# Kernel tuning notes

Hardware: AMD Instinct MI355X
Metric: run time of the kernel (lower is better)

Reference implementation:

```python
import jax, jax.numpy as jnp
import numpy as np

B, T, NF, C = 4, 512, 65, 128
NH, E, H, DOWN, L = 4, 8, 256, 4, 100
VD = C // NH

def _ln(x, g, b, eps=1e-5):
    m = x.mean(-1, keepdims=True)
    v = ((x - m) ** 2).mean(-1, keepdims=True)
    return (x - m) / jnp.sqrt(v + eps) * g + b

def _prelu(x, a):
    return jnp.where(x >= 0, x, a * x)

def _lstm(x, h0, c0, wih, whh, bih, bhh):
    # x: [N, S, D] -> ([N, S, H], hT, cT); PyTorch gate order i,f,g,o
    xp = x @ wih.T + (bih + bhh)
    def step(carry, xt):
        h, c = carry
        g = xt + h @ whh.T
        i, f, gg, o = jnp.split(g, 4, axis=-1)
        c = jax.nn.sigmoid(f) * c + jax.nn.sigmoid(i) * jnp.tanh(gg)
        h = jax.nn.sigmoid(o) * jnp.tanh(c)
        return (h, c), h
    (hT, cT), ys = jax.lax.scan(step, (h0, c0), xp.transpose(1, 0, 2))
    return ys.transpose(1, 0, 2), hT, cT

def setup_inputs():
    key = jax.random.key(0)
    ks = iter(jax.random.split(key, 64))
    def w(*shape):
        return (jax.random.normal(next(ks), shape) * 0.05).astype(jnp.float32)
    z = lambda *s: jnp.zeros(s, jnp.float32)
    o = lambda *s: jnp.ones(s, jnp.float32)
    a = jnp.float32(0.25)  # PReLU init
    return dict(
        x=jax.random.normal(next(ks), (B, T, NF, C), jnp.float32),
        conv_w=w(C, C, DOWN), conv_b=z(C), conv_a=a, ln0_g=o(C), ln0_b=z(C),
        iwih_f=w(4*H, C), iwhh_f=w(4*H, H), ibih_f=z(4*H), ibhh_f=z(4*H),
        iwih_r=w(4*H, C), iwhh_r=w(4*H, H), ibih_r=z(4*H), ibhh_r=z(4*H),
        deconv_w=w(2*H, C, DOWN), deconv_b=z(C),
        ln1_g=o(C), ln1_b=z(C),
        wih=w(4*H, C), whh=w(4*H, H), bih=z(4*H), bhh=z(4*H),
        lin_w=w(C, H), lin_b=z(C),
        q_w=w(E*NH, C), q_b=z(E*NH), q_a=a, q_lg=o(NF*E), q_lb=z(NF*E),
        k_w=w(E*NH, C), k_b=z(E*NH), k_a=a, k_lg=o(NF*E), k_lb=z(NF*E),
        v_w=w(VD*NH, C), v_b=z(VD*NH), v_a=a, v_lg=o(NF*VD), v_lb=z(NF*VD),
        p_w=w(C, C), p_b=z(C), p_a=a, p_lg=o(NF*C), p_lb=z(NF*C),
        K_buf=z(B*NH, L-1, NF*E), V_buf=z(B*NH, L-1, NF*VD),
        h0=z(B*NF, H), c0=z(B*NF, H),
    )

def reference(x, conv_w, conv_b, conv_a, ln0_g, ln0_b,
              iwih_f, iwhh_f, ibih_f, ibhh_f, iwih_r, iwhh_r, ibih_r, ibhh_r,
              deconv_w, deconv_b, ln1_g, ln1_b, wih, whh, bih, bhh, lin_w, lin_b,
              q_w, q_b, q_a, q_lg, q_lb, k_w, k_b, k_a, k_lg, k_lb,
              v_w, v_b, v_a, v_lg, v_lb, p_w, p_b, p_a, p_lg, p_lb,
              K_buf, V_buf, h0, c0):
    Qd = NF // DOWN
    BT = B * T
    # ---- intra: Conv1d(k=s=DOWN) -> PReLU -> LN -> BiLSTM over freq -> ConvTranspose1d, residual ----
    # k == s: conv is a blocked einsum; torch drops the trailing NF - Qd*DOWN samples
    xc = x.reshape(BT, NF, C)[:, :Qd*DOWN, :].reshape(BT, Qd, DOWN, C)
    h = _prelu(jnp.einsum('nimc,ocm->nio', xc, conv_w) + conv_b, conv_a)
    h = _ln(h, ln0_g, ln0_b)
    z0 = jnp.zeros((BT, H), x.dtype)
    yf, _, _ = _lstm(h, z0, z0, iwih_f, iwhh_f, ibih_f, ibhh_f)
    yr, _, _ = _lstm(h[:, ::-1], z0, z0, iwih_r, iwhh_r, ibih_r, ibhh_r)
    hbi = jnp.concatenate([yf, yr[:, ::-1]], -1)                      # [BT, Qd, 2H]
    # ConvTranspose1d with k == s: blocked einsum; output_padding fills zeros (+bias) at the end
    zz = jnp.einsum('nid,dom->nimo', hbi, deconv_w).reshape(BT, Qd*DOWN, C)
    zz = jnp.pad(zz, ((0, 0), (0, NF - Qd*DOWN), (0, 0))) + deconv_b
    intra = zz.reshape(B, T, NF, C) + x
    # ---- inter: LN -> causal LSTM over time with carried (h0, c0) -> Linear, residual ----
    y = _ln(intra, ln1_g, ln1_b).transpose(0, 2, 1, 3).reshape(B*NF, T, C)
    ys, _, _ = _lstm(y, h0, c0, wih, whh, bih, bhh)
    y = (ys @ lin_w.T + lin_b).reshape(B, NF, T, C).transpose(0, 2, 1, 3)
    inter = y + intra
    # ---- causal sliding-window MHA with streaming K/V buffers ----
    def qkv(w_, b_, a_, lg_, lb_, d):
        hh = _prelu(jnp.einsum('btqc,dc->btqd', inter, w_) + b_, a_)
        hh = hh.reshape(B, T, NF, NH, d).transpose(0, 3, 1, 2, 4).reshape(B*NH, T, NF*d)
        return _ln(hh, lg_, lb_)
    Qh = qkv(q_w, q_b, q_a, q_lg, q_lb, E)      # [B*NH, T, NF*E]
    Kh = qkv(k_w, k_b, k_a, k_lg, k_lb, E)
    Vh = qkv(v_w, v_b, v_a, v_lg, v_lb, VD)     # [B*NH, T, NF*VD]
    Kf = jnp.concatenate([K_buf, Kh], 1)        # [B*NH, T+L-1, NF*E]
    Vf = jnp.concatenate([V_buf, Vh], 1)
    scores = jnp.einsum('bte,bse->bts', Qh, Kf) / jnp.asarray(NF*E, x.dtype)**0.5
    tq = jnp.arange(T)[:, None]
    tk = jnp.arange(T + L - 1)[None, :]
    band = (tk >= tq) & (tk < tq + L)           # window of L keys ending at frame t
    probs = jax.nn.softmax(jnp.where(band, scores, -jnp.inf), -1)
    av = jnp.einsum('bts,bsv->btv', probs, Vf)
    av = av.reshape(B, NH, T, NF, VD).transpose(0, 2, 3, 1, 4).reshape(B, T, NF, C)
    ph = _prelu(jnp.einsum('btqc,dc->btqd', av, p_w) + p_b, p_a)
    ph = _ln(ph.reshape(B, T, NF*C), p_lg, p_lb).reshape(B, T, NF, C)
    return ph + inter
```

## Files before the change

### kernel.cpp

```cpp
#include <hip/hip_runtime.h>
#include <hip/hip_bf16.h>


typedef unsigned short u16;
typedef unsigned int u32;

#define OFF_A    0ULL
#define OFF_B    68157440ULL
#define OFF_C    136314880ULL
#define OFF_DE   204472320ULL
#define OFF_WT   238551040ULL

__device__ __forceinline__ float b2f(u16 u) {
  union { u32 i; float f; } v; v.i = ((u32)u) << 16; return v.f;
}
__device__ __forceinline__ float bflo(u32 u) {
  union { u32 i; float f; } v; v.i = u << 16; return v.f;
}
__device__ __forceinline__ float bfhi(u32 u) {
  union { u32 i; float f; } v; v.i = u & 0xffff0000u; return v.f;
}
__device__ __forceinline__ float sigf(float x) { return 1.f / (1.f + __expf(-x)); }
__device__ __forceinline__ float tanh_(float x) {
  float cx = fminf(15.f, fmaxf(-15.f, x));
  float e = __expf(2.f * cx);
  return (e - 1.f) / (e + 1.f);
}
__device__ __forceinline__ void wavered2(float& s, float& q) {
  #pragma unroll
  for (int o = 32; o > 0; o >>= 1) {
    s += __shfl_down(s, o, 64);
    q += __shfl_down(q, o, 64);
  }
}

__global__ void k_transpose_ff(const float* __restrict__ src, float* __restrict__ dst,
                               int R, int K) {
  int e = blockIdx.x * 256 + threadIdx.x;
  if (e >= R * K) return;
  int r = e / K, k = e - r * K;
  dst[k * R + r] = src[e];
}

__global__ void k_transpose_fb(const float* __restrict__ src, u16* __restrict__ dst,
                               int R, int K) {
  int e = blockIdx.x * 256 + threadIdx.x;
  if (e >= R * K) return;
  int r = e / K, k = e - r * K;
  __hip_bfloat16 h = __float2bfloat16(src[e]);
  dst[k * R + r] = *(u16*)&h;
}

__global__ void k_cast_fb(const float* __restrict__ src, u16* __restrict__ dst, int n) {
  int e = blockIdx.x * 256 + threadIdx.x;
  if (e >= n) return;
  __hip_bfloat16 h = __float2bfloat16(src[e]);
  dst[e] = *(u16*)&h;
}

__global__ __launch_bounds__(256) void k_conv_ln0(
    const float* __restrict__ x32, const float* __restrict__ cw,
    const float* __restrict__ cb, const float* __restrict__ ca,
    const float* __restrict__ g0, const float* __restrict__ b0,
    float* __restrict__ hc) {
  __shared__ float xs[8192];
  __shared__ float hs[2048];
  __shared__ float mu_[16], ri_[16];
  int n = blockIdx.x, tid = threadIdx.x;
  const float4* xr = (const float4*)(x32 + (size_t)n * 8320);
  for (int e = tid; e < 2048; e += 256) ((float4*)xs)[e] = xr[e];
  __syncthreads();
  int g = tid >> 7, o = tid & 127;
  float a = ca[0];
  float cbv = cb[o];
  float acc[8];
  #pragma unroll
  for (int j = 0; j < 8; ++j) acc[j] = cbv;
  const float4* cw4 = (const float4*)cw;
  for (int c = 0; c < 128; ++c) {
    float4 w = cw4[o * 128 + c];
    #pragma unroll
    for (int j = 0; j < 8; ++j) {
      int i = 8 * g + j;
      const float* xi = &xs[i * 512 + c];
      acc[j] += w.x * xi[0] + w.y * xi[128] + w.z * xi[256] + w.w * xi[384];
    }
  }
  #pragma unroll
  for (int j = 0; j < 8; ++j) {
    int i = 8 * g + j;
    float v = acc[j];
    v = v >= 0.f ? v : a * v;
    hs[i * 128 + o] = v;
  }
  __syncthreads();
  if (tid < 16) {
    float s = 0.f, q = 0.f;
    for (int c = 0; c < 128; ++c) { float v = hs[tid * 128 + c]; s += v; q += v * v; }
    float mu = s / 128.f;
    mu_[tid] = mu;
    ri_[tid] = rsqrtf(fmaxf(q / 128.f - mu * mu, 0.f) + 1e-5f);
  }
  __syncthreads();
  float gg = g0[o], bb = b0[o];
  #pragma unroll
  for (int j = 0; j < 8; ++j) {
    int i = 8 * g + j;
    hc[((size_t)n * 16 + i) * 128 + o] = (hs[i * 128 + o] - mu_[i]) * ri_[i] * gg + bb;
  }
}

__global__ __launch_bounds__(256) void k_intra_lstm(
    const float* __restrict__ hc,
    const float* __restrict__ wiTf, const float* __restrict__ whTf,
    const float* __restrict__ bihf, const float* __restrict__ bhhf,
    const float* __restrict__ wiTr, const float* __restrict__ whTr,
    const float* __restrict__ bihr, const float* __restrict__ bhhr,
    float* __restrict__ yf, float* __restrict__ yr) {
  __shared__ float xt[1024];
  __shared__ float hsh[2048];
  __shared__ float csh[2048];
  __shared__ float gbuf[8192];
  int tid = threadIdx.x;
  int grp = blockIdx.x & 255, dir = blockIdx.x >> 8;
  int n0 = grp * 8;
  const float4* wi4 = (const float4*)(dir ? wiTr : wiTf);
  const float4* wh4 = (const float4*)(dir ? whTr : whTf);
  const float* bi = dir ? bihr : bihf;
  const float* bh = dir ? bhhr : bhhf;
  float* yo = dir ? yr : yf;
  float bias[4];
  #pragma unroll
  for (int j = 0; j < 4; ++j) bias[j] = bi[4 * tid + j] + bh[4 * tid + j];
  for (int e = tid; e < 2048; e += 256) { hsh[e] = 0.f; csh[e] = 0.f; }
  for (int t = 0; t < 16; ++t) {
    int tt = dir ? 15 - t : t;
    for (int e = tid; e < 1024; e += 256)
      xt[e] = hc[((size_t)(n0 + (e >> 7)) * 16 + tt) * 128 + (e & 127)];
    __syncthreads();
    float acc[4][8];
    #pragma unroll
    for (int j = 0; j < 4; ++j)
      #pragma unroll
      for (int s = 0; s < 8; ++s) acc[j][s] = bias[j];
    for (int k = 0; k < 128; ++k) {
      float4 w = wi4[k * 256 + tid];
      #pragma unroll
      for (int s = 0; s < 8; ++s) {
        float xv = xt[s * 128 + k];
        acc[0][s] += w.x * xv; acc[1][s] += w.y * xv;
        acc[2][s] += w.z * xv; acc[3][s] += w.w * xv;
      }
    }
    for (int k = 0; k < 256; ++k) {
      float4 w = wh4[k * 256 + tid];
      #pragma unroll
      for (int s = 0; s < 8; ++s) {
        float hv = hsh[s * 256 + k];
        acc[0][s] += w.x * hv; acc[1][s] += w.y * hv;
        acc[2][s] += w.z * hv; acc[3][s] += w.w * hv;
      }
    }
    #pragma unroll
    for (int j = 0; j < 4; ++j)
      #pragma unroll
      for (int s = 0; s < 8; ++s)
        gbuf[s * 1024 + 4 * tid + j] = acc[j][s];
    __syncthreads();
    #pragma unroll
    for (int s = 0; s < 8; ++s) {
      float iv = gbuf[s * 1024 + tid];
      float fv = gbuf[s * 1024 + 256 + tid];
      float gv = gbuf[s * 1024 + 512 + tid];
      float ov = gbuf[s * 1024 + 768 + tid];
      float cn = sigf(fv) * csh[s * 256 + tid] + sigf(iv) * tanh_(gv);
      float hn = sigf(ov) * tanh_(cn);
      csh[s * 256 + tid] = cn;
      hsh[s * 256 + tid] = hn;
      yo[((size_t)(n0 + s) * 16 + tt) * 256 + tid] = hn;
    }
    __syncthreads();
  }
}

__global__ __launch_bounds__(256) void k_deconv(
    const float* __restrict__ yf, const float* __restrict__ yr,
    const float* __restrict__ dw, const float* __restrict__ db,
    const float* __restrict__ x32, float* __restrict__ intra) {
  __shared__ float hbi[8192];
  int n = blockIdx.x, tid = threadIdx.x;
  for (int e = tid; e < 8192; e += 256) {
    int i = e >> 9, d = e & 511;
    hbi[e] = d < 256 ? yf[((size_t)n * 16 + i) * 256 + d]
                     : yr[((size_t)n * 16 + i) * 256 + d - 256];
  }
  __syncthreads();
  int op0 = tid, op1 = tid + 256;
  float acc0[16], acc1[16];
  #pragma unroll
  for (int i = 0; i < 16; ++i) { acc0[i] = 0.f; acc1[i] = 0.f; }
  for (int d = 0; d < 512; d += 2) {
    float w00 = dw[(size_t)d * 512 + op0];
    float w01 = dw[(size_t)d * 512 + op1];
    float w10 = dw[(size_t)(d + 1) * 512 + op0];
    float w11 = dw[(size_t)(d + 1) * 512 + op1];
    #pragma unroll
    for (int i = 0; i < 16; ++i) {
      float2 hv = *(const float2*)&hbi[i * 512 + d];
      acc0[i] += hv.x * w00 + hv.y * w10;
      acc1[i] += hv.x * w01 + hv.y * w11;
    }
  }
  int o0 = op0 >> 2, m0 = op0 & 3, o1 = op1 >> 2, m1 = op1 & 3;
  float db0 = db[o0], db1 = db[o1];
  #pragma unroll
  for (int i = 0; i < 16; ++i) {
    size_t i0 = ((size_t)n * 65 + i * 4 + m0) * 128 + o0;
    size_t i1 = ((size_t)n * 65 + i * 4 + m1) * 128 + o1;
    intra[i0] = acc0[i] + db0 + x32[i0];
    intra[i1] = acc1[i] + db1 + x32[i1];
  }
  if (tid < 128) {
    size_t ip = ((size_t)n * 65 + 64) * 128 + tid;
    intra[ip] = db[tid] + x32[ip];
  }
}

__global__ __launch_bounds__(256) void k_ln1(
    const float* __restrict__ intra, const float* __restrict__ g1,
    const float* __restrict__ b1, float* __restrict__ out) {
  __shared__ float rs[4], rq[4];
  int n = blockIdx.x, tid = threadIdx.x;
  int gr = tid >> 7, o = tid & 127, wid = tid >> 6;
  int b = n >> 9, t = n & 511;
  float gv = g1[o], bv = b1[o];
  for (int f0 = 0; f0 < 65; f0 += 2) {
    int f = f0 + gr;
    bool ok = f < 65;
    float v = 0.f;
    if (ok) v = intra[((size_t)n * 65 + f) * 128 + o];
    float s = v, q = v * v;
    wavered2(s, q);
    if ((tid & 63) == 0) { rs[wid] = s; rq[wid] = q; }
    __syncthreads();
    if (ok) {
      float S = rs[2 * gr] + rs[2 * gr + 1], Q = rq[2 * gr] + rq[2 * gr + 1];
      float mu = S / 128.f;
      float rinv = rsqrtf(fmaxf(Q / 128.f - mu * mu, 0.f) + 1e-5f);
      out[((size_t)(b * 65 + f) * 512 + t) * 128 + o] = (v - mu) * rinv * gv + bv;
    }
    __syncthreads();
  }
}

__global__ __launch_bounds__(1024, 4) void k_inter_lstm(
    const float* __restrict__ ln1y,
    const u16* __restrict__ wiTb, const u16* __restrict__ whTb,
    const float* __restrict__ bih, const float* __restrict__ bhh,
    const u16* __restrict__ lwb, const float* __restrict__ lb,
    const float* __restrict__ h0a, const float* __restrict__ c0a,
    const float* __restrict__ intra, float* __restrict__ inter) {
  __shared__ float xt2[128][2];
  __shared__ float hs2[256][2];
  __shared__ float cs2[256][2];
  __shared__ float pb[8][2][1024];
  int tid = threadIdx.x;
  int n0 = blockIdx.x * 2;
  if (tid < 512) {
    int s = tid >> 8, j = tid & 255;
    hs2[j][s] = h0a[(size_t)(n0 + s) * 256 + j];
    cs2[j][s] = c0a[(size_t)(n0 + s) * 256 + j];
  }
  int g = tid >> 7, l = tid & 127;
  int s3 = tid >> 8, j3 = tid & 255;
  float bi_i = 0.f, bi_f = 0.f, bi_g = 0.f, bi_o = 0.f;
  if (tid < 512) {
    bi_i = bih[j3] + bhh[j3];
    bi_f = bih[256 + j3] + bhh[256 + j3];
    bi_g = bih[512 + j3] + bhh[512 + j3];
    bi_o = bih[768 + j3] + bhh[768 + j3];
  }
  int s5 = tid >> 7, c5 = tid & 127;
  int n_l = n0 + s5;
  int b_l = n_l / 65, f_l = n_l - b_l * 65;
  float linb = (tid < 256) ? lb[c5] : 0.f;
  int c4 = tid >> 3, part8 = tid & 7;
  const u16* lwp = lwb + (size_t)c4 * 256 + part8 * 32;
  const u16* wip = wiTb + (size_t)(g * 16) * 1024 + l * 8;
  const u16* whp = whTb + (size_t)(g * 32) * 1024 + l * 8;
  int kx0 = g * 16, kh0 = g * 32;
  __syncthreads();
  for (int t = 0; t < 512; ++t) {
    float resid = 0.f;
    size_t oi = 0;
    if (tid < 256) {
      float xv = __builtin_nontemporal_load(
          &ln1y[(size_t)n_l * 65536 + (size_t)t * 128 + c5]);
      xt2[c5][s5] = xv;
      oi = ((size_t)(b_l * 512 + t) * 65 + f_l) * 128 + c5;
      resid = __builtin_nontemporal_load(&intra[oi]);
    }
    __syncthreads();
    float a[16];
    #pragma unroll
    for (int i = 0; i < 16; ++i) a[i] = 0.f;
    #pragma unroll 4
    for (int k = 0; k < 16; ++k) {
      uint4 u = *(const uint4*)(wip + (size_t)k * 1024);
      float2 xv = *(const float2*)xt2[kx0 + k];
      float w0 = bflo(u.x), w1 = bfhi(u.x), w2 = bflo(u.y), w3 = bfhi(u.y);
      float w4 = bflo(u.z), w5 = bfhi(u.z), w6 = bflo(u.w), w7 = bfhi(u.w);
      a[0] += w0 * xv.x; a[1] += w1 * xv.x; a[2] += w2 * xv.x; a[3] += w3 * xv.x;
      a[4] += w4 * xv.x; a[5] += w5 * xv.x; a[6] += w6 * xv.x; a[7] += w7 * xv.x;
      a[8] += w0 * xv.y; a[9] += w1 * xv.y; a[10] += w2 * xv.y; a[11] += w3 * xv.y;
      a[12] += w4 * xv.y; a[13] += w5 * xv.y; a[14] += w6 * xv.y; a[15] += w7 * xv.y;
    }
    #pragma unroll 4
    for (int k = 0; k < 32; ++k) {
      uint4 u = *(const uint4*)(whp + (size_t)k * 1024);
      float2 hv = *(const float2*)hs2[kh0 + k];
      float w0 = bflo(u.x), w1 = bfhi(u.x), w2 = bflo(u.y), w3 = bfhi(u.y);
      float w4 = bflo(u.z), w5 = bfhi(u.z), w6 = bflo(u.w), w7 = bfhi(u.w);
      a[0] += w0 * hv.x; a[1] += w1 * hv.x; a[2] += w2 * hv.x; a[3] += w3 * hv.x;
      a[4] += w4 * hv.x; a[5] += w5 * hv.x; a[6] += w6 * hv.x; a[7] += w7 * hv.x;
      a[8] += w0 * hv.y; a[9] += w1 * hv.y; a[10] += w2 * hv.y; a[11] += w3 * hv.y;
      a[12] += w4 * hv.y; a[13] += w5 * hv.y; a[14] += w6 * hv.y; a[15] += w7 * hv.y;
    }
    *(float4*)&pb[g][0][l * 8]     = make_float4(a[0], a[1], a[2], a[3]);
    *(float4*)&pb[g][0][l * 8 + 4] = make_float4(a[4], a[5], a[6], a[7]);
    *(float4*)&pb[g][1][l * 8]     = make_float4(a[8], a[9], a[10], a[11]);
    *(float4*)&pb[g][1][l * 8 + 4] = make_float4(a[12], a[13], a[14], a[15]);
    __syncthreads();
    if (tid < 512) {
      float iv = bi_i, fv = bi_f, gv = bi_g, ov = bi_o;
      #pragma unroll
      for (int g2 = 0; g2 < 8; ++g2) {
        iv += pb[g2][s3][j3];
        fv += pb[g2][s3][256 + j3];
        gv += pb[g2][s3][512 + j3];
        ov += pb[g2][s3][768 + j3];
      }
      float cn = sigf(fv) * cs2[j3][s3] + sigf(iv) * tanh_(gv);
      float hn = sigf(ov) * tanh_(cn);
      cs2[j3][s3] = cn;
      hs2[j3][s3] = hn;
    }
    __syncthreads();
    {
      float p0 = 0.f, p1 = 0.f;
      #pragma unroll
      for (int j = 0; j < 8; ++j) {
        int ch = (j + part8) & 7;
        uint2 u = *(const uint2*)(lwp + ch * 4);
        int k = part8 * 32 + ch * 4;
        float2 h0 = *(const float2*)hs2[k];
        float2 h1 = *(const float2*)hs2[k + 1];
        float2 h2 = *(const float2*)hs2[k + 2];
        float2 h3 = *(const float2*)hs2[k + 3];
        float w0 = bflo(u.x), w1 = bfhi(u.x), w2 = bflo(u.y), w3 = bfhi(u.y);
        p0 += w0 * h0.x + w1 * h1.x + w2 * h2.x + w3 * h3.x;
        p1 += w0 * h0.y + w1 * h1.y + w2 * h2.y + w3 * h3.y;
      }
      pb[0][0][c4 * 8 + part8] = p0;
      pb[0][1][c4 * 8 + part8] = p1;
    }
    __syncthreads();
    if (tid < 256) {
      const float4* pp = (const float4*)&pb[0][s5][c5 * 8];
      float4 q0 = pp[0], q1 = pp[1];
      float acc = linb + resid + q0.x + q0.y + q0.z + q0.w
                               + q1.x + q1.y + q1.z + q1.w;
      __builtin_nontemporal_store(acc, &inter[oi]);
    }
  }
}

__global__ __launch_bounds__(256) void k_qkv(
    const float* __restrict__ inter,
    const float* __restrict__ qw, const float* __restrict__ qb, const float* __restrict__ qa,
    const float* __restrict__ kw, const float* __restrict__ kb, const float* __restrict__ ka,
    const float* __restrict__ vw, const float* __restrict__ vb, const float* __restrict__ va,
    float* __restrict__ Qh, float* __restrict__ Kh, float* __restrict__ Vh) {
  __shared__ float xsl[8320];
  int n = blockIdx.x, tid = threadIdx.x;
  int b = n >> 9, t = n & 511;
  for (int e = tid; e < 8320; e += 256) xsl[e] = inter[(size_t)n * 8320 + e];
  __syncthreads();
  if (tid >= 192) return;
  const float* wrow; float bias, a; float* dst; int dsz;
  if (tid < 32) {
    wrow = qw + (size_t)tid * 128; bias = qb[tid]; a = qa[0];
    dst = Qh + ((size_t)(b * 4 + (tid >> 3)) * 512 + t) * 520 + (tid & 7); dsz = 8;
  } else if (tid < 64) {
    int d = tid - 32;
    wrow = kw + (size_t)d * 128; bias = kb[d]; a = ka[0];
    dst = Kh + ((size_t)(b * 4 + (d >> 3)) * 512 + t) * 520 + (d & 7); dsz = 8;
  } else {
    int d = tid - 64;
    wrow = vw + (size_t)d * 128; bias = vb[d]; a = va[0];
    dst = Vh + ((size_t)(b * 4 + (d >> 5)) * 512 + t) * 2080 + (d & 31); dsz = 32;
  }
  const float4* w4 = (const float4*)wrow;
  for (int f = 0; f < 65; ++f) {
    float acc = bias;
    const float4* xr = (const float4*)&xsl[f * 128];
    #pragma unroll
    for (int kk = 0; kk < 32; ++kk) {
      float4 w = w4[kk], xv = xr[kk];
      acc += w.x * xv.x + w.y * xv.y + w.z * xv.z + w.w * xv.w;
    }
    acc = acc >= 0.f ? acc : a * acc;
    dst[(size_t)f * dsz] = acc;
  }
}

__global__ __launch_bounds__(256) void k_lnrow(
    float* __restrict__ buf, int len,
    const float* __restrict__ g, const float* __restrict__ b) {
  __shared__ float rs[4], rq[4];
  int row = blockIdx.x, tid = threadIdx.x;
  float* p = buf + (size_t)row * len;
  float s = 0.f, q = 0.f;
  for (int e = tid; e < len; e += 256) { float v = p[e]; s += v; q += v * v; }
  wavered2(s, q);
  if ((tid & 63) == 0) { rs[tid >> 6] = s; rq[tid >> 6] = q; }
  __syncthreads();
  float S = rs[0] + rs[1] + rs[2] + rs[3];
  float Q = rq[0] + rq[1] + rq[2] + rq[3];
  float mu = S / len;
  float rinv = rsqrtf(fmaxf(Q / len - mu * mu, 0.f) + 1e-5f);
  for (int e = tid; e < len; e += 256) {
    float v = p[e];
    p[e] = (v - mu) * rinv * g[e] + b[e];
  }
}

__global__ __launch_bounds__(256) void k_attn(
    const float* __restrict__ Qh, const float* __restrict__ Kh,
    const float* __restrict__ Vh, const float* __restrict__ Kbuf,
    const float* __restrict__ Vbuf, float* __restrict__ av) {
  __shared__ float qrow[520], sc[100], red[2];
  int bid = blockIdx.x, tid = threadIdx.x;
  int bh = bid >> 9, t = bid & 511;
  for (int e = tid; e < 520; e += 256)
    qrow[e] = Qh[((size_t)bh * 512 + t) * 520 + e];
  __syncthreads();
  if (tid < 100) {
    int s = t + tid;
    float acc = 0.f;
    if (s < 99) {
      const float* kr = Kbuf + ((size_t)bh * 99 + s) * 520;
      for (int e = 0; e < 520; ++e) acc += qrow[e] * kr[e];
    } else {
      const float* kr = Kh + ((size_t)bh * 512 + (s - 99)) * 520;
      for (int e = 0; e < 520; ++e) acc += qrow[e] * kr[e];
    }
    sc[tid] = acc * 0.04385290096535147f;
  }
  __syncthreads();
  if (tid == 0) {
    float m = sc[0];
    for (int k = 1; k < 100; ++k) m = fmaxf(m, sc[k]);
    red[0] = m;
  }
  __syncthreads();
  if (tid < 100) sc[tid] = __expf(sc[tid] - red[0]);
  __syncthreads();
  if (tid == 0) {
    float s = 0.f;
    for (int k = 0; k < 100; ++k) s += sc[k];
    red[1] = 1.f / s;
  }
  __syncthreads();
  float rscale = red[1];
  int b = bh >> 2, nh = bh & 3;
  int kb = t < 99 ? 99 - t : 0;
  for (int o = tid; o < 2080; o += 256) {
    float acc = 0.f;
    for (int k = 0; k < kb; ++k)
      acc += sc[k] * Vbuf[((size_t)bh * 99 + t + k) * 2080 + o];
    for (int k = kb; k < 100; ++k)
      acc += sc[k] * Vh[((size_t)bh * 512 + (t + k - 99)) * 2080 + o];
    int f = o >> 5, vd = o & 31;
    av[((size_t)(b * 512 + t) * 65 + f) * 128 + nh * 32 + vd] = acc * rscale;
  }
}

__global__ __launch_bounds__(256) void k_pproj(
    const float* __restrict__ av, const float* __restrict__ pw,
    const float* __restrict__ pb, const float* __restrict__ pa,
    float* __restrict__ ph) {
  __shared__ float avs[8320];
  int n = blockIdx.x, tid = threadIdx.x;
  for (int e = tid; e < 8320; e += 256) avs[e] = av[(size_t)n * 8320 + e];
  __syncthreads();
  int o = tid & 127, g = tid >> 7;
  float a = pa[0], bias = pb[o];
  const float4* w4 = (const float4*)(pw + (size_t)o * 128);
  for (int f = g; f < 65; f += 2) {
    float acc = bias;
    const float4* xr = (const float4*)&avs[f * 128];
    #pragma unroll
    for (int kk = 0; kk < 32; ++kk) {
      float4 w = w4[kk], xv = xr[kk];
      acc += w.x * xv.x + w.y * xv.y + w.z * xv.z + w.w * xv.w;
    }
    acc = acc >= 0.f ? acc : a * acc;
    ph[(size_t)n * 8320 + f * 128 + o] = acc;
  }
}

__global__ __launch_bounds__(256) void k_lnfinal(
    const float* __restrict__ ph, const float* __restrict__ plg,
    const float* __restrict__ plb, const float* __restrict__ inter,
    float* __restrict__ out) {
  __shared__ float rs[4], rq[4];
  int n = blockIdx.x, tid = threadIdx.x;
  const float* p = ph + (size_t)n * 8320;
  float s = 0.f, q = 0.f;
  for (int e = tid; e < 8320; e += 256) { float v = p[e]; s += v; q += v * v; }
  wavered2(s, q);
  if ((tid & 63) == 0) { rs[tid >> 6] = s; rq[tid >> 6] = q; }
  __syncthreads();
  float S = rs[0] + rs[1] + rs[2] + rs[3];
  float Q = rq[0] + rq[1] + rq[2] + rq[3];
  float mu = S / 8320.f;
  float rinv = rsqrtf(fmaxf(Q / 8320.f - mu * mu, 0.f) + 1e-5f);
  for (int e = tid; e < 8320; e += 256) {
    out[(size_t)n * 8320 + e] =
        (p[e] - mu) * rinv * plg[e] + plb[e] + inter[(size_t)n * 8320 + e];
  }
}

extern "C" void kernel_launch(void* const* d_in, const int* in_sizes, int n_in,
                              void* d_out, int out_size, void* d_ws, size_t ws_size,
                              hipStream_t stream) {
  const float* x       = (const float*)d_in[0];
  const float* conv_w  = (const float*)d_in[1];
  const float* conv_b  = (const float*)d_in[2];
  const float* conv_a  = (const float*)d_in[3];
  const float* ln0_g   = (const float*)d_in[4];
  const float* ln0_b   = (const float*)d_in[5];
  const float* iwih_f  = (const float*)d_in[6];
  const float* iwhh_f  = (const float*)d_in[7];
  const float* ibih_f  = (const float*)d_in[8];
  const float* ibhh_f  = (const float*)d_in[9];
  const float* iwih_r  = (const float*)d_in[10];
  const float* iwhh_r  = (const float*)d_in[11];
  const float* ibih_r  = (const float*)d_in[12];
  const float* ibhh_r  = (const float*)d_in[13];
  const float* deconv_w= (const float*)d_in[14];
  const float* deconv_b= (const float*)d_in[15];
  const float* ln1_g   = (const float*)d_in[16];
  const float* ln1_b   = (const float*)d_in[17];
  const float* wih     = (const float*)d_in[18];
  const float* whh     = (const float*)d_in[19];
  const float* bih     = (const float*)d_in[20];
  const float* bhh     = (const float*)d_in[21];
  const float* lin_w   = (const float*)d_in[22];
  const float* lin_b   = (const float*)d_in[23];
  const float* q_w     = (const float*)d_in[24];
  const float* q_b     = (const float*)d_in[25];
  const float* q_a     = (const float*)d_in[26];
  const float* q_lg    = (const float*)d_in[27];
  const float* q_lb    = (const float*)d_in[28];
  const float* k_w     = (const float*)d_in[29];
  const float* k_b     = (const float*)d_in[30];
  const float* k_a     = (const float*)d_in[31];
  const float* k_lg    = (const float*)d_in[32];
  const float* k_lb    = (const float*)d_in[33];
  const float* v_w     = (const float*)d_in[34];
  const float* v_b     = (const float*)d_in[35];
  const float* v_a     = (const float*)d_in[36];
  const float* v_lg    = (const float*)d_in[37];
  const float* v_lb    = (const float*)d_in[38];
  const float* p_w     = (const float*)d_in[39];
  const float* p_b     = (const float*)d_in[40];
  const float* p_a     = (const float*)d_in[41];
  const float* p_lg    = (const float*)d_in[42];
  const float* p_lb    = (const float*)d_in[43];
  const float* K_buf   = (const float*)d_in[44];
  const float* V_buf   = (const float*)d_in[45];
  const float* h0v     = (const float*)d_in[46];
  const float* c0v     = (const float*)d_in[47];

  char* ws = (char*)d_ws;
  float* hc    = (float*)(ws + OFF_A);
  float* yfb   = (float*)(ws + OFF_A + 16777216ULL);
  float* yrb   = (float*)(ws + OFF_DE);
  float* ln1y  = (float*)(ws + OFF_A);
  float* Vh    = (float*)(ws + OFF_A);
  float* phb   = (float*)(ws + OFF_A);
  float* intra = (float*)(ws + OFF_B);
  float* avb   = (float*)(ws + OFF_B);
  float* inter = (float*)(ws + OFF_C);
  float* Qh    = (float*)(ws + OFF_DE);
  float* Kh    = (float*)(ws + OFF_DE + 17039360ULL);
  float* wT    = (float*)(ws + OFF_WT);
  float* wiTf = wT + 0;
  float* whTf = wT + 131072;
  float* wiTr = wT + 393216;
  float* whTr = wT + 524288;
  u16* wiTb = (u16*)(wT + 786432);
  u16* whTb = wiTb + 131072;
  u16* lwb  = whTb + 262144;

  k_transpose_ff<<<512, 256, 0, stream>>>(iwih_f, wiTf, 1024, 128);
  k_transpose_ff<<<1024, 256, 0, stream>>>(iwhh_f, whTf, 1024, 256);
  k_transpose_ff<<<512, 256, 0, stream>>>(iwih_r, wiTr, 1024, 128);
  k_transpose_ff<<<1024, 256, 0, stream>>>(iwhh_r, whTr, 1024, 256);
  k_transpose_fb<<<512, 256, 0, stream>>>(wih, wiTb, 1024, 128);
  k_transpose_fb<<<1024, 256, 0, stream>>>(whh, whTb, 1024, 256);
  k_cast_fb<<<128, 256, 0, stream>>>(lin_w, lwb, 32768);

  k_conv_ln0<<<2048, 256, 0, stream>>>(x, conv_w, conv_b, conv_a, ln0_g, ln0_b, hc);
  k_intra_lstm<<<512, 256, 0, stream>>>(hc, wiTf, whTf, ibih_f, ibhh_f,
                                        wiTr, whTr, ibih_r, ibhh_r, yfb, yrb);
  k_deconv<<<2048, 256, 0, stream>>>(yfb, yrb, deconv_w, deconv_b, x, intra);
  k_ln1<<<2048, 256, 0, stream>>>(intra, ln1_g, ln1_b, ln1y);
  k_inter_lstm<<<130, 1024, 0, stream>>>(ln1y, wiTb, whTb, bih, bhh,
                                         lwb, lin_b, h0v, c0v, intra, inter);
  k_qkv<<<2048, 256, 0, stream>>>(inter, q_w, q_b, q_a, k_w, k_b, k_a,
                                  v_w, v_b, v_a, Qh, Kh, Vh);
  k_lnrow<<<8192, 256, 0, stream>>>(Qh, 520, q_lg, q_lb);
  k_lnrow<<<8192, 256, 0, stream>>>(Kh, 520, k_lg, k_lb);
  k_lnrow<<<8192, 256, 0, stream>>>(Vh, 2080, v_lg, v_lb);
  k_attn<<<8192, 256, 0, stream>>>(Qh, Kh, Vh, K_buf, V_buf, avb);
  k_pproj<<<2048, 256, 0, stream>>>(avb, p_w, p_b, p_a, phb);
  k_lnfinal<<<2048, 256, 0, stream>>>(phb, p_lg, p_lb, inter, (float*)d_out);
}
```

Before: 6.995 ms.

## Move inter-frame LSTM recurrence onto bf16 MFMA with split hi/lo activations

Rewrites the inter-frame LSTM kernel so each block handles 16 sequences and computes the gate GEMM and output linear with 16x16x32 bf16 MFMA instructions. Weights are pre-packed into MFMA fragment layout. Activations are split into hi and lo bf16 parts to keep close to fp32 accuracy. Next-step inputs are prefetched into double-buffered LDS, which removes several barriers per step. The trade-off is that the grid shrinks from 130 blocks to 17, so far fewer CUs are used, and the extra lo-part MFMAs double the matrix work.

```diff
diff --git a/kernel.cpp b/kernel.cpp
--- a/kernel.cpp
+++ b/kernel.cpp
@@ -11,8 +11,16 @@
 #define OFF_DE   204472320ULL
 #define OFF_WT   238551040ULL
 
+typedef __attribute__((ext_vector_type(8))) short bf16x8;
+typedef __attribute__((ext_vector_type(4))) float f32x4;
+
 __device__ __forceinline__ float b2f(u16 u) {
   union { u32 i; float f; } v; v.i = ((u32)u) << 16; return v.f;
+}
+__device__ __forceinline__ u16 f2b(float f) {
+  union { float f; u32 i; } v; v.f = f;
+  u32 r = v.i + 0x7fffu + ((v.i >> 16) & 1u);
+  return (u16)(r >> 16);
 }
 __device__ __forceinline__ float bflo(u32 u) {
   union { u32 i; float f; } v; v.i = u << 16; return v.f;
@@ -42,20 +50,28 @@
   dst[k * R + r] = src[e];
 }
 
-__global__ void k_transpose_fb(const float* __restrict__ src, u16* __restrict__ dst,
-                               int R, int K) {
-  int e = blockIdx.x * 256 + threadIdx.x;
-  if (e >= R * K) return;
-  int r = e / K, k = e - r * K;
-  __hip_bfloat16 h = __float2bfloat16(src[e]);
-  dst[k * R + r] = *(u16*)&h;
-}
-
-__global__ void k_cast_fb(const float* __restrict__ src, u16* __restrict__ dst, int n) {
-  int e = blockIdx.x * 256 + threadIdx.x;
-  if (e >= n) return;
-  __hip_bfloat16 h = __float2bfloat16(src[e]);
-  dst[e] = *(u16*)&h;
+__global__ void k_prep_gfrag(const float* __restrict__ wih, const float* __restrict__ whh,
+                             u16* __restrict__ dst) {
+  int idx = blockIdx.x * 256 + threadIdx.x;
+  if (idx >= 393216) return;
+  int j = idx & 7, l = (idx >> 3) & 63;
+  int r3 = idx >> 9;
+  int kc = r3 % 12, nt = r3 / 12;
+  int k = kc * 32 + ((l >> 4) << 3) + j;
+  int n = (nt << 4) + (l & 15);
+  float v = k < 128 ? wih[(size_t)n * 128 + k] : whh[(size_t)n * 256 + (k - 128)];
+  dst[idx] = f2b(v);
+}
+
+__global__ void k_prep_lfrag(const float* __restrict__ lw, u16* __restrict__ dst) {
+  int idx = blockIdx.x * 256 + threadIdx.x;
+  if (idx >= 32768) return;
+  int j = idx & 7, l = (idx >> 3) & 63;
+  int r3 = idx >> 9;
+  int kc = r3 & 7, nt = r3 >> 3;
+  int k = kc * 32 + ((l >> 4) << 3) + j;
+  int n = (nt << 4) + (l & 15);
+  dst[idx] = f2b(lw[(size_t)n * 256 + k]);
 }
 
 __global__ __launch_bounds__(256) void k_conv_ln0(
@@ -253,125 +269,152 @@
   }
 }
 
-__global__ __launch_bounds__(1024, 4) void k_inter_lstm(
+__global__ __launch_bounds__(512, 2) void k_inter_lstm(
     const float* __restrict__ ln1y,
-    const u16* __restrict__ wiTb, const u16* __restrict__ whTb,
+    const u16* __restrict__ gfrag, const u16* __restrict__ lfrag,
     const float* __restrict__ bih, const float* __restrict__ bhh,
-    const u16* __restrict__ lwb, const float* __restrict__ lb,
+    const float* __restrict__ lb,
     const float* __restrict__ h0a, const float* __restrict__ c0a,
     const float* __restrict__ intra, float* __restrict__ inter) {
-  __shared__ float xt2[128][2];
-  __shared__ float hs2[256][2];
-  __shared__ float cs2[256][2];
-  __shared__ float pb[8][2][1024];
+  __shared__ __align__(16) u16 Ahi[2][6144];
+  __shared__ __align__(16) u16 Alo[2][6144];
   int tid = threadIdx.x;
-  int n0 = blockIdx.x * 2;
-  if (tid < 512) {
-    int s = tid >> 8, j = tid & 255;
-    hs2[j][s] = h0a[(size_t)(n0 + s) * 256 + j];
-    cs2[j][s] = c0a[(size_t)(n0 + s) * 256 + j];
-  }
-  int g = tid >> 7, l = tid & 127;
-  int s3 = tid >> 8, j3 = tid & 255;
-  float bi_i = 0.f, bi_f = 0.f, bi_g = 0.f, bi_o = 0.f;
-  if (tid < 512) {
-    bi_i = bih[j3] + bhh[j3];
-    bi_f = bih[256 + j3] + bhh[256 + j3];
-    bi_g = bih[512 + j3] + bhh[512 + j3];
-    bi_o = bih[768 + j3] + bhh[768 + j3];
-  }
-  int s5 = tid >> 7, c5 = tid & 127;
-  int n_l = n0 + s5;
-  int b_l = n_l / 65, f_l = n_l - b_l * 65;
-  float linb = (tid < 256) ? lb[c5] : 0.f;
-  int c4 = tid >> 3, part8 = tid & 7;
-  const u16* lwp = lwb + (size_t)c4 * 256 + part8 * 32;
-  const u16* wip = wiTb + (size_t)(g * 16) * 1024 + l * 8;
-  const u16* whp = whTb + (size_t)(g * 32) * 1024 + l * 8;
-  int kx0 = g * 16, kh0 = g * 32;
-  __syncthreads();
+  int w = tid >> 6, l = tid & 63;
+  int n0 = blockIdx.x * 16;
+  int r0 = (l >> 4) << 2;
+  int cl = l & 15;
+
+  int skc  = tid >> 7;
+  int sl   = (tid & 127) >> 1;
+  int sj   = (tid & 1) << 2;
+  int srow = sl & 15;
+  int sk   = skc * 32 + ((sl >> 4) << 3) + sj;
+  int sseq = n0 + srow;
+  bool sok = sseq < 260;
+  const float4* xsrc =
+      (const float4*)(ln1y + (size_t)(sok ? sseq : 0) * 65536 + sk);
+  int sdst = skc * 512 + sl * 8 + sj;
+
+  float bsum[4][2];
+  #pragma unroll
+  for (int g = 0; g < 4; ++g)
+    #pragma unroll
+    for (int m = 0; m < 2; ++m) {
+      int col = 256 * g + 32 * w + 16 * m + cl;
+      bsum[g][m] = bih[col] + bhh[col];
+    }
+  float lbv = lb[16 * w + cl];
+
+  bool rok[4];
+  size_t rbase[4];
+  #pragma unroll
+  for (int reg = 0; reg < 4; ++reg) {
+    int seq = n0 + r0 + reg;
+    rok[reg] = seq < 260;
+    int sq = rok[reg] ? seq : 0;
+    int b_ = sq / 65, f_ = sq - b_ * 65;
+    rbase[reg] = ((size_t)b_ * 512 * 65 + f_) * 128 + 16 * w + cl;
+  }
+
+  float cst[2][4];
+  #pragma unroll
+  for (int m = 0; m < 2; ++m) {
+    int col = 32 * w + 16 * m + cl;
+    #pragma unroll
+    for (int reg = 0; reg < 4; ++reg) {
+      int seq = n0 + r0 + reg;
+      float c0v_ = (seq < 260) ? c0a[(size_t)seq * 256 + col] : 0.f;
+      float h0v_ = (seq < 260) ? h0a[(size_t)seq * 256 + col] : 0.f;
+      cst[m][reg] = c0v_;
+      u16 hh = f2b(h0v_);
+      u16 hl = f2b(h0v_ - b2f(hh));
+      int idx = (4 + w) * 512 + ((r0 + reg) + 16 * (2 * m + (cl >> 3))) * 8 + (l & 7);
+      Ahi[0][idx] = hh; Alo[0][idx] = hl;
+    }
+  }
+  {
+    float4 xv = sok ? xsrc[0] : make_float4(0.f, 0.f, 0.f, 0.f);
+    u16 a0 = f2b(xv.x), a1 = f2b(xv.y), a2 = f2b(xv.z), a3 = f2b(xv.w);
+    u16 c0_ = f2b(xv.x - b2f(a0)), c1_ = f2b(xv.y - b2f(a1)),
+        c2_ = f2b(xv.z - b2f(a2)), c3_ = f2b(xv.w - b2f(a3));
+    *(uint2*)&Ahi[0][sdst] =
+        make_uint2((u32)a0 | ((u32)a1 << 16), (u32)a2 | ((u32)a3 << 16));
+    *(uint2*)&Alo[0][sdst] =
+        make_uint2((u32)c0_ | ((u32)c1_ << 16), (u32)c2_ | ((u32)c3_ << 16));
+  }
+  __syncthreads();
+
   for (int t = 0; t < 512; ++t) {
-    float resid = 0.f;
-    size_t oi = 0;
-    if (tid < 256) {
-      float xv = __builtin_nontemporal_load(
-          &ln1y[(size_t)n_l * 65536 + (size_t)t * 128 + c5]);
-      xt2[c5][s5] = xv;
-      oi = ((size_t)(b_l * 512 + t) * 65 + f_l) * 128 + c5;
-      resid = __builtin_nontemporal_load(&intra[oi]);
+    const u16* phi = Ahi[t & 1];
+    const u16* plo = Alo[t & 1];
+    u16* qhi = Ahi[(t + 1) & 1];
+    u16* qlo = Alo[(t + 1) & 1];
+    int tn = t < 511 ? t + 1 : 511;
+    float4 xv = sok ? xsrc[(size_t)tn * 32] : make_float4(0.f, 0.f, 0.f, 0.f);
+    float rsd[4];
+    #pragma unroll
+    for (int reg = 0; reg < 4; ++reg)
+      rsd[reg] = rok[reg]
+          ? __builtin_nontemporal_load(&intra[rbase[reg] + (size_t)t * 8320])
+          : 0.f;
+
+    f32x4 acc[4][2];
+    #pragma unroll
+    for (int g = 0; g < 4; ++g)
+      #pragma unroll
+      for (int m = 0; m < 2; ++m)
+        acc[g][m] = (f32x4){bsum[g][m], bsum[g][m], bsum[g][m], bsum[g][m]};
+    #pragma unroll 3
+    for (int kc = 0; kc < 12; ++kc) {
+      bf16x8 ah = *(const bf16x8*)&phi[kc * 512 + l * 8];
+      bf16x8 al = *(const bf16x8*)&plo[kc * 512 + l * 8];
+      #pragma unroll
+      for (int g = 0; g < 4; ++g)
+        #pragma unroll
+        for (int m = 0; m < 2; ++m) {
+          int nt = 16 * g + 2 * w + m;
+          bf16x8 bw = *(const bf16x8*)&gfrag[(size_t)(nt * 12 + kc) * 512 + l * 8];
+          acc[g][m] = __builtin_amdgcn_mfma_f32_16x16x32_bf16(ah, bw, acc[g][m], 0, 0, 0);
+          acc[g][m] = __builtin_amdgcn_mfma_f32_16x16x32_bf16(al, bw, acc[g][m], 0, 0, 0);
+        }
+    }
+    #pragma unroll
+    for (int m = 0; m < 2; ++m) {
+      #pragma unroll
+      for (int reg = 0; reg < 4; ++reg) {
+        float iv = acc[0][m][reg], fv = acc[1][m][reg];
+        float gv = acc[2][m][reg], ov = acc[3][m][reg];
+        float cn = sigf(fv) * cst[m][reg] + sigf(iv) * tanh_(gv);
+        float hn = sigf(ov) * tanh_(cn);
+        cst[m][reg] = cn;
+        u16 hh = f2b(hn);
+        u16 hl = f2b(hn - b2f(hh));
+        int idx = (4 + w) * 512 + ((r0 + reg) + 16 * (2 * m + (cl >> 3))) * 8 + (l & 7);
+        qhi[idx] = hh; qlo[idx] = hl;
+      }
+    }
+    {
+      u16 a0 = f2b(xv.x), a1 = f2b(xv.y), a2 = f2b(xv.z), a3 = f2b(xv.w);
+      u16 c0_ = f2b(xv.x - b2f(a0)), c1_ = f2b(xv.y - b2f(a1)),
+          c2_ = f2b(xv.z - b2f(a2)), c3_ = f2b(xv.w - b2f(a3));
+      *(uint2*)&qhi[sdst] =
+          make_uint2((u32)a0 | ((u32)a1 << 16), (u32)a2 | ((u32)a3 << 16));
+      *(uint2*)&qlo[sdst] =
+          make_uint2((u32)c0_ | ((u32)c1_ << 16), (u32)c2_ | ((u32)c3_ << 16));
     }
     __syncthreads();
-    float a[16];
-    #pragma unroll
-    for (int i = 0; i < 16; ++i) a[i] = 0.f;
-    #pragma unroll 4
-    for (int k = 0; k < 16; ++k) {
-      uint4 u = *(const uint4*)(wip + (size_t)k * 1024);
-      float2 xv = *(const float2*)xt2[kx0 + k];
-      float w0 = bflo(u.x), w1 = bfhi(u.x), w2 = bflo(u.y), w3 = bfhi(u.y);
-      float w4 = bflo(u.z), w5 = bfhi(u.z), w6 = bflo(u.w), w7 = bfhi(u.w);
-      a[0] += w0 * xv.x; a[1] += w1 * xv.x; a[2] += w2 * xv.x; a[3] += w3 * xv.x;
-      a[4] += w4 * xv.x; a[5] += w5 * xv.x; a[6] += w6 * xv.x; a[7] += w7 * xv.x;
-      a[8] += w0 * xv.y; a[9] += w1 * xv.y; a[10] += w2 * xv.y; a[11] += w3 * xv.y;
-      a[12] += w4 * xv.y; a[13] += w5 * xv.y; a[14] += w6 * xv.y; a[15] += w7 * xv.y;
-    }
-    #pragma unroll 4
-    for (int k = 0; k < 32; ++k) {
-      uint4 u = *(const uint4*)(whp + (size_t)k * 1024);
-      float2 hv = *(const float2*)hs2[kh0 + k];
-      float w0 = bflo(u.x), w1 = bfhi(u.x), w2 = bflo(u.y), w3 = bfhi(u.y);
-      float w4 = bflo(u.z), w5 = bfhi(u.z), w6 = bflo(u.w), w7 = bfhi(u.w);
-      a[0] += w0 * hv.x; a[1] += w1 * hv.x; a[2] += w2 * hv.x; a[3] += w3 * hv.x;
-      a[4] += w4 * hv.x; a[5] += w5 * hv.x; a[6] += w6 * hv.x; a[7] += w7 * hv.x;
-      a[8] += w0 * hv.y; a[9] += w1 * hv.y; a[10] += w2 * hv.y; a[11] += w3 * hv.y;
-      a[12] += w4 * hv.y; a[13] += w5 * hv.y; a[14] += w6 * hv.y; a[15] += w7 * hv.y;
-    }
-    *(float4*)&pb[g][0][l * 8]     = make_float4(a[0], a[1], a[2], a[3]);
-    *(float4*)&pb[g][0][l * 8 + 4] = make_float4(a[4], a[5], a[6], a[7]);
-    *(float4*)&pb[g][1][l * 8]     = make_float4(a[8], a[9], a[10], a[11]);
-    *(float4*)&pb[g][1][l * 8 + 4] = make_float4(a[12], a[13], a[14], a[15]);
-    __syncthreads();
-    if (tid < 512) {
-      float iv = bi_i, fv = bi_f, gv = bi_g, ov = bi_o;
-      #pragma unroll
-      for (int g2 = 0; g2 < 8; ++g2) {
-        iv += pb[g2][s3][j3];
-        fv += pb[g2][s3][256 + j3];
-        gv += pb[g2][s3][512 + j3];
-        ov += pb[g2][s3][768 + j3];
-      }
-      float cn = sigf(fv) * cs2[j3][s3] + sigf(iv) * tanh_(gv);
-      float hn = sigf(ov) * tanh_(cn);
-      cs2[j3][s3] = cn;
-      hs2[j3][s3] = hn;
-    }
-    __syncthreads();
-    {
-      float p0 = 0.f, p1 = 0.f;
-      #pragma unroll
-      for (int j = 0; j < 8; ++j) {
-        int ch = (j + part8) & 7;
-        uint2 u = *(const uint2*)(lwp + ch * 4);
-        int k = part8 * 32 + ch * 4;
-        float2 h0 = *(const float2*)hs2[k];
-        float2 h1 = *(const float2*)hs2[k + 1];
-        float2 h2 = *(const float2*)hs2[k + 2];
-        float2 h3 = *(const float2*)hs2[k + 3];
-        float w0 = bflo(u.x), w1 = bfhi(u.x), w2 = bflo(u.y), w3 = bfhi(u.y);
-        p0 += w0 * h0.x + w1 * h1.x + w2 * h2.x + w3 * h3.x;
-        p1 += w0 * h0.y + w1 * h1.y + w2 * h2.y + w3 * h3.y;
-      }
-      pb[0][0][c4 * 8 + part8] = p0;
-      pb[0][1][c4 * 8 + part8] = p1;
-    }
-    __syncthreads();
-    if (tid < 256) {
-      const float4* pp = (const float4*)&pb[0][s5][c5 * 8];
-      float4 q0 = pp[0], q1 = pp[1];
-      float acc = linb + resid + q0.x + q0.y + q0.z + q0.w
-                               + q1.x + q1.y + q1.z + q1.w;
-      __builtin_nontemporal_store(acc, &inter[oi]);
-    }
+    f32x4 lacc = (f32x4){0.f, 0.f, 0.f, 0.f};
+    #pragma unroll
+    for (int kc = 0; kc < 8; ++kc) {
+      bf16x8 ah = *(const bf16x8*)&qhi[(4 + kc) * 512 + l * 8];
+      bf16x8 bw = *(const bf16x8*)&lfrag[(size_t)(w * 8 + kc) * 512 + l * 8];
+      lacc = __builtin_amdgcn_mfma_f32_16x16x32_bf16(ah, bw, lacc, 0, 0, 0);
+    }
+    #pragma unroll
+    for (int reg = 0; reg < 4; ++reg)
+      if (rok[reg])
+        __builtin_nontemporal_store(lacc[reg] + lbv + rsd[reg],
+                                    &inter[rbase[reg] + (size_t)t * 8320]);
   }
 }
 
@@ -601,25 +644,23 @@
   float* whTf = wT + 131072;
   float* wiTr = wT + 393216;
   float* whTr = wT + 524288;
-  u16* wiTb = (u16*)(wT + 786432);
-  u16* whTb = wiTb + 131072;
-  u16* lwb  = whTb + 262144;
+  u16* gfragW = (u16*)(wT + 786432);
+  u16* lfragW = gfragW + 393216;
 
   k_transpose_ff<<<512, 256, 0, stream>>>(iwih_f, wiTf, 1024, 128);
   k_transpose_ff<<<1024, 256, 0, stream>>>(iwhh_f, whTf, 1024, 256);
   k_transpose_ff<<<512, 256, 0, stream>>>(iwih_r, wiTr, 1024, 128);
   k_transpose_ff<<<1024, 256, 0, stream>>>(iwhh_r, whTr, 1024, 256);
-  k_transpose_fb<<<512, 256, 0, stream>>>(wih, wiTb, 1024, 128);
-  k_transpose_fb<<<1024, 256, 0, stream>>>(whh, whTb, 1024, 256);
-  k_cast_fb<<<128, 256, 0, stream>>>(lin_w, lwb, 32768);
+  k_prep_gfrag<<<1536, 256, 0, stream>>>(wih, whh, gfragW);
+  k_prep_lfrag<<<128, 256, 0, stream>>>(lin_w, lfragW);
 
   k_conv_ln0<<<2048, 256, 0, stream>>>(x, conv_w, conv_b, conv_a, ln0_g, ln0_b, hc);
   k_intra_lstm<<<512, 256, 0, stream>>>(hc, wiTf, whTf, ibih_f, ibhh_f,
                                         wiTr, whTr, ibih_r, ibhh_r, yfb, yrb);
   k_deconv<<<2048, 256, 0, stream>>>(yfb, yrb, deconv_w, deconv_b, x, intra);
   k_ln1<<<2048, 256, 0, stream>>>(intra, ln1_g, ln1_b, ln1y);
-  k_inter_lstm<<<130, 1024, 0, stream>>>(ln1y, wiTb, whTb, bih, bhh,
-                                         lwb, lin_b, h0v, c0v, intra, inter);
+  k_inter_lstm<<<17, 512, 0, stream>>>(ln1y, gfragW, lfragW, bih, bhh,
+                                       lin_b, h0v, c0v, intra, inter);
   k_qkv<<<2048, 256, 0, stream>>>(inter, q_w, q_b, q_a, k_w, k_b, k_a,
                                   v_w, v_b, v_a, Qh, Kh, Vh);
   k_lnrow<<<8192, 256, 0, stream>>>(Qh, 520, q_lg, q_lb);
```

New measurement: 10.43 ms. +49.1%, slower.
